# Kernel tuning notes

Hardware: AMD Instinct MI355X
Metric: run time of the kernel (lower is better)

The kernel has to match this reference:

```python
import jax, jax.numpy as jnp
import numpy as np

N_NODES = 100000
N_EDGES = 1600000
D_IN = 64
D_HID = 64
D_OUT = 64


def setup_inputs() -> dict:
    key = jax.random.key(0)
    ks = jax.random.split(key, 12)
    x = jax.random.normal(ks[0], (N_NODES, D_IN), dtype=jnp.float32)
    edge_index = jax.random.randint(ks[1], (2, N_EDGES), 0, N_NODES, dtype=jnp.int64)
    def lin(k, fan_in, fan_out):
        s = 1.0 / np.sqrt(fan_in)
        return jax.random.uniform(k, (fan_out, fan_in), jnp.float32, -s, s)
    dims = [(D_IN, D_HID), (D_HID, D_HID), (D_HID, D_OUT)]
    params = {}
    for i, (di, do) in enumerate(dims):
        params[f"W_l{i}"] = lin(ks[2 + 3 * i], di, do)      # weight for aggregated neighbors
        params[f"W_r{i}"] = lin(ks[3 + 3 * i], di, do)      # weight for root/self features
        params[f"b{i}"] = jnp.zeros((do,), jnp.float32)
    return {"x": x, "edge_index": edge_index, **params}


def _sage_conv(x, src, dst, W_l, W_r, b):
    # mean aggregation of source features at destination nodes
    agg = jax.ops.segment_sum(x[src], dst, num_segments=N_NODES)          # [N, d]
    cnt = jax.ops.segment_sum(jnp.ones_like(dst, dtype=x.dtype), dst, num_segments=N_NODES)
    mean = agg / jnp.maximum(cnt, 1.0)[:, None]
    return mean @ W_l.T + x @ W_r.T + b


def reference(x, edge_index, W_l0, W_r0, b0, W_l1, W_r1, b1, W_l2, W_r2, b2):
    src, dst = edge_index[0], edge_index[1]
    h = jax.nn.relu(_sage_conv(x, src, dst, W_l0, W_r0, b0))
    h = jax.nn.relu(_sage_conv(h, src, dst, W_l1, W_r1, b1))
    out = _sage_conv(h, src, dst, W_l2, W_r2, b2)
    return out
```

## Files before the change

### kernel.cpp

```cpp
#include <hip/hip_runtime.h>

#define N_NODES 100000
#define N_EDGES 1600000
#define D 64
#define NB 131
#define NBUCKETS 764
#define PCHUNK 8192
#define NCHUNK 196
#define PBLK 1024

typedef unsigned int u32;
typedef unsigned short u16;
typedef _Float16 f16;
typedef f16 f16x8 __attribute__((ext_vector_type(8)));
typedef float f32x4 __attribute__((ext_vector_type(4)));

__global__ __launch_bounds__(PBLK) void hist_kernel(const int* __restrict__ dst,
                                                    int* __restrict__ hist) {
    __shared__ int hcnt[NBUCKETS];
    int t = threadIdx.x;
    int c0 = blockIdx.x * PCHUNK;
    int nloc = min(PCHUNK, N_EDGES - c0);
    for (int i = t; i < NBUCKETS; i += PBLK) hcnt[i] = 0;
    __syncthreads();
    for (int i = t; i < nloc; i += PBLK) atomicAdd(&hcnt[dst[c0 + i] / NB], 1);
    __syncthreads();
    for (int i = t; i < NBUCKETS; i += PBLK) hist[blockIdx.x * NBUCKETS + i] = hcnt[i];
}

__global__ __launch_bounds__(1024) void cscan_kernel(int* __restrict__ hist,
                                                     int* __restrict__ bptr) {
    __shared__ int s[1024];
    int t = threadIdx.x;
    int tot = 0;
    if (t < NBUCKETS)
        for (int c = 0; c < NCHUNK; ++c) tot += hist[c * NBUCKETS + t];
    s[t] = tot;
    __syncthreads();
    for (int off = 1; off < 1024; off <<= 1) {
        int a = (t >= off) ? s[t - off] : 0;
        __syncthreads();
        s[t] += a;
        __syncthreads();
    }
    if (t < NBUCKETS) {
        int run = s[t] - tot;
        bptr[t] = run;
        for (int c = 0; c < NCHUNK; ++c) {
            int v = hist[c * NBUCKETS + t];
            hist[c * NBUCKETS + t] = run;
            run += v;
        }
    }
    if (t == NBUCKETS - 1) bptr[NBUCKETS] = s[t];
}

__global__ __launch_bounds__(PBLK) void part_kernel(const int* __restrict__ src,
                                                    const int* __restrict__ dst,
                                                    const int* __restrict__ cbase,
                                                    u32* __restrict__ pairs) {
    __shared__ int hcur[NBUCKETS];
    __shared__ int hb[NBUCKETS];
    int t = threadIdx.x;
    int c0 = blockIdx.x * PCHUNK;
    int nloc = min(PCHUNK, N_EDGES - c0);
    for (int i = t; i < NBUCKETS; i += PBLK) {
        hcur[i] = 0;
        hb[i] = cbase[blockIdx.x * NBUCKETS + i];
    }
    __syncthreads();
    for (int i = t; i < nloc; i += PBLK) {
        int s = src[c0 + i];
        int d = dst[c0 + i];
        int b = d / NB;
        int r = atomicAdd(&hcur[b], 1);
        pairs[hb[b] + r] = ((u32)(d - b * NB) << 24) | (u32)s;
    }
}

__global__ __launch_bounds__(256) void local_csr_kernel(
    const u32* __restrict__ pairs, const int* __restrict__ bptr,
    int* __restrict__ row_ptr, int* __restrict__ cnt, float* __restrict__ inv,
    int* __restrict__ csr_src)
{
    __shared__ int lcnt[NB];
    __shared__ int lofs[NB];
    __shared__ int s[256];

    int t = threadIdx.x, b = blockIdx.x;
    int e0 = bptr[b], e1 = bptr[b + 1];
    int nb0 = b * NB;

    for (int i = t; i < NB; i += 256) lcnt[i] = 0;
    __syncthreads();
    for (int e = e0 + t; e < e1; e += 256) atomicAdd(&lcnt[pairs[e] >> 24], 1);
    __syncthreads();

    int v = (t < NB) ? lcnt[t] : 0;
    s[t] = v;
    __syncthreads();
    for (int off = 1; off < 256; off <<= 1) {
        int a = (t >= off) ? s[t - off] : 0;
        __syncthreads();
        s[t] += a;
        __syncthreads();
    }
    if (t < NB) {
        int node = nb0 + t;
        if (node < N_NODES) {
            int excl = s[t] - v;
            lofs[t] = excl;
            row_ptr[node] = e0 + excl;
            cnt[node] = v;
            inv[node] = 1.0f / fmaxf((float)v, 1.0f);
        }
        lcnt[t] = 0;
    }
    __syncthreads();
    for (int e = e0 + t; e < e1; e += 256) {
        u32 p = pairs[e];
        int dl = (int)(p >> 24);
        int pos = atomicAdd(&lcnt[dl], 1);
        csr_src[e0 + lofs[dl] + pos] = (int)(p & 0xFFFFFFu);
    }
}

__global__ void tof16_kernel(const float* __restrict__ in, u16* __restrict__ outh, int n4) {
    int i = blockIdx.x * blockDim.x + threadIdx.x;
    if (i < n4) {
        float4 v = reinterpret_cast<const float4*>(in)[i];
        union { f16 h[4]; uint2 u; } cv;
        cv.h[0] = (f16)v.x; cv.h[1] = (f16)v.y; cv.h[2] = (f16)v.z; cv.h[3] = (f16)v.w;
        reinterpret_cast<uint2*>(outh)[i] = cv.u;
    }
}

__global__ void prep_bfrag(const float* __restrict__ Wl0, const float* __restrict__ Wr0,
                           const float* __restrict__ Wl1, const float* __restrict__ Wr1,
                           const float* __restrict__ Wl2, const float* __restrict__ Wr2,
                           uint4* __restrict__ Bfrag) {
    int idx = blockIdx.x * blockDim.x + threadIdx.x;
    if (idx >= 3 * 16 * 64) return;
    int layer = idx >> 10, r = idx & 1023, f = r >> 6, l = r & 63;
    const float* Wl = layer == 0 ? Wl0 : layer == 1 ? Wl1 : Wl2;
    const float* Wr = layer == 0 ? Wr0 : layer == 1 ? Wr1 : Wr2;
    int ktg = f >> 2, nt = f & 3;
    const float* W = (ktg & 2) ? Wr : Wl;
    int o = nt * 16 + (l & 15);
    int k = (ktg & 1) * 32 + (l >> 4) * 8;
    const float* s = W + o * 64 + k;
    float4 v0 = *reinterpret_cast<const float4*>(s);
    float4 v1 = *reinterpret_cast<const float4*>(s + 4);
    union { f16x8 h; uint4 u; } cv;
    cv.h[0] = (f16)v0.x; cv.h[1] = (f16)v0.y; cv.h[2] = (f16)v0.z; cv.h[3] = (f16)v0.w;
    cv.h[4] = (f16)v1.x; cv.h[5] = (f16)v1.y; cv.h[6] = (f16)v1.z; cv.h[7] = (f16)v1.w;
    Bfrag[idx] = cv.u;
}

__device__ __forceinline__ void add8(float* va, uint4 r) {
    union { uint4 u; f16x8 h; } cv; cv.u = r;
    #pragma unroll
    for (int e = 0; e < 8; ++e) va[e] += (float)cv.h[e];
}

__global__ __launch_bounds__(256, 8) void sage_layer(
    const u16* __restrict__ hh,
    const int* __restrict__ row_ptr, const int* __restrict__ cnt,
    const int* __restrict__ csr_src, const float* __restrict__ inv,
    const uint4* __restrict__ Bfrag,
    const float* __restrict__ bvec,
    float* __restrict__ outf,
    u16* __restrict__ outh,
    int relu)
{
    __shared__ u16 Atile[4][16][128];

    int t = threadIdx.x;
    int w    = t >> 6;
    int lane = t & 63;
    int j8   = lane & 7;
    int sg   = lane >> 3;
    const uint4* rows = reinterpret_cast<const uint4*>(hh);

    int base = blockIdx.x * 64 + w * 16;

    float bias[4];
    #pragma unroll
    for (int nt = 0; nt < 4; ++nt) bias[nt] = bvec[nt * 16 + (lane & 15)];

    #pragma unroll
    for (int slot = 0; slot < 2; ++slot) {
        int n = slot * 8 + sg;
        int node = base + n;
        bool valid = node < N_NODES;
        int nodec = valid ? node : N_NODES - 1;
        uint4 selfrow = rows[nodec * 8 + j8];
        int s0 = row_ptr[nodec];
        int c  = valid ? cnt[nodec] : 0;
        float va[8] = {0.f,0.f,0.f,0.f,0.f,0.f,0.f,0.f};
        int j = 0;
        int i0 = 0, i1 = 0, i2 = 0, i3 = 0;
        bool have = (c >= 4);
        if (have) {
            i0 = csr_src[s0];     i1 = csr_src[s0 + 1];
            i2 = csr_src[s0 + 2]; i3 = csr_src[s0 + 3];
        }
        while (have) {
            uint4 r0 = rows[i0 * 8 + j8];
            uint4 r1 = rows[i1 * 8 + j8];
            uint4 r2 = rows[i2 * 8 + j8];
            uint4 r3 = rows[i3 * 8 + j8];
            j += 4;
            have = (j + 4 <= c);
            if (have) {
                i0 = csr_src[s0 + j];     i1 = csr_src[s0 + j + 1];
                i2 = csr_src[s0 + j + 2]; i3 = csr_src[s0 + j + 3];
            }
            add8(va, r0); add8(va, r1); add8(va, r2); add8(va, r3);
        }
        for (; j < c; ++j) {
            add8(va, rows[csr_src[s0 + j] * 8 + j8]);
        }
        float sc = inv[nodec];
        union { f16x8 h; uint4 u; } mv;
        #pragma unroll
        for (int e = 0; e < 8; ++e) mv.h[e] = (f16)(va[e] * sc);
        int chunk = j8 ^ (n & 7);
        if (valid) {
            *reinterpret_cast<uint4*>(&Atile[w][n][chunk * 8]) = mv.u;
            *reinterpret_cast<uint4*>(&Atile[w][n][64 + chunk * 8]) = selfrow;
        }
    }

    f32x4 acc[4] = {};
    int row = lane & 15, kg = lane >> 4;
    #pragma unroll
    for (int ktg = 0; ktg < 4; ++ktg) {
        int idx16 = ktg * 4 + kg;
        int swz = (idx16 & 8) | ((idx16 & 7) ^ (row & 7));
        uint4 a = *reinterpret_cast<const uint4*>(&Atile[w][row][swz * 8]);
        union { uint4 u; f16x8 h; } av; av.u = a;
        #pragma unroll
        for (int nt = 0; nt < 4; ++nt) {
            union { uint4 u; f16x8 h; } bv; bv.u = Bfrag[(ktg * 4 + nt) * 64 + lane];
            acc[nt] = __builtin_amdgcn_mfma_f32_16x16x32_f16(av.h, bv.h, acc[nt], 0, 0, 0);
        }
    }

    #pragma unroll
    for (int nt = 0; nt < 4; ++nt) {
        int o = nt * 16 + (lane & 15);
        #pragma unroll
        for (int r = 0; r < 4; ++r) {
            int n = kg * 4 + r;
            int node = base + n;
            if (node < N_NODES) {
                float vout = acc[nt][r] + bias[nt];
                if (relu) vout = fmaxf(vout, 0.f);
                if (outf) outf[node * 64 + o] = vout;
                if (outh) {
                    union { f16 h; u16 u; } cv; cv.h = (f16)vout;
                    outh[node * 64 + o] = cv.u;
                }
            }
        }
    }
}

extern "C" void kernel_launch(void* const* d_in, const int* in_sizes, int n_in,
                              void* d_out, int out_size, void* d_ws, size_t ws_size,
                              hipStream_t stream) {
    const float* x   = (const float*)d_in[0];
    const int*   ei  = (const int*)d_in[1];
    const int*   src = ei;
    const int*   dst = ei + N_EDGES;
    const float* Wl0 = (const float*)d_in[2];
    const float* Wr0 = (const float*)d_in[3];
    const float* b0  = (const float*)d_in[4];
    const float* Wl1 = (const float*)d_in[5];
    const float* Wr1 = (const float*)d_in[6];
    const float* b1  = (const float*)d_in[7];
    const float* Wl2 = (const float*)d_in[8];
    const float* Wr2 = (const float*)d_in[9];
    const float* b2  = (const float*)d_in[10];
    float* out = (float*)d_out;

    char* p = (char*)d_ws;
    auto take = [&](size_t bytes) { char* r = p; p += (bytes + 255) & ~(size_t)255; return r; };
    int*   hist    = (int*)take((size_t)NCHUNK * NBUCKETS * 4);
    int*   bptr    = (int*)take((size_t)(NBUCKETS + 1) * 4);
    u32*   pairs   = (u32*)take((size_t)N_EDGES * 4);
    int*   csr_src = (int*)take((size_t)N_EDGES * 4);
    int*   row_ptr = (int*)take((size_t)N_NODES * 4);
    int*   cnt     = (int*)take((size_t)N_NODES * 4);
    float* inv     = (float*)take((size_t)N_NODES * 4);
    uint4* Bfrag   = (uint4*)take((size_t)3 * 16 * 64 * 16);
    u16*   xh      = (u16*)take((size_t)N_NODES * D * 2);
    u16*   h0h     = (u16*)take((size_t)N_NODES * D * 2);
    u16*   h1h     = (u16*)take((size_t)N_NODES * D * 2);

    const int BLK = 256;
    const int conv_grid  = (N_NODES * D / 4 + BLK - 1) / BLK;
    const int layer_grid = (N_NODES + 63) / 64;

    hist_kernel<<<NCHUNK, PBLK, 0, stream>>>(dst, hist);
    cscan_kernel<<<1, 1024, 0, stream>>>(hist, bptr);
    part_kernel<<<NCHUNK, PBLK, 0, stream>>>(src, dst, hist, pairs);
    local_csr_kernel<<<NBUCKETS, BLK, 0, stream>>>(pairs, bptr, row_ptr, cnt, inv, csr_src);
    tof16_kernel<<<conv_grid, BLK, 0, stream>>>(x, xh, N_NODES * D / 4);
    prep_bfrag<<<(3 * 1024 + BLK - 1) / BLK, BLK, 0, stream>>>(Wl0, Wr0, Wl1, Wr1, Wl2, Wr2, Bfrag);

    sage_layer<<<layer_grid, BLK, 0, stream>>>(xh,  row_ptr, cnt, csr_src, inv, Bfrag,        b0, nullptr, h0h, 1);
    sage_layer<<<layer_grid, BLK, 0, stream>>>(h0h, row_ptr, cnt, csr_src, inv, Bfrag + 1024, b1, nullptr, h1h, 1);
    sage_layer<<<layer_grid, BLK, 0, stream>>>(h1h, row_ptr, cnt, csr_src, inv, Bfrag + 2048, b2, out, nullptr, 0);
}
```

Measured before the change: 182.8 us.

## Interleave two nodes' neighbor gathers per lane and split scan into three kernels

Each lane now gathers neighbor rows for both of its nodes in one loop instead of one node after the other, so twice as many loads are in flight and memory latency is better hidden. Occupancy is lowered from 8 to 6 waves per SIMD to make room for the extra registers. The single-block column scan is split into a column-sum kernel, a bucket scan and a rebase kernel so the sums spread across several blocks, at the cost of two extra launches. Lanes whose two nodes have different degrees may leave some slots idle, and the lower occupancy could offset the gain.

```diff
diff --git a/kernel.cpp b/kernel.cpp
--- a/kernel.cpp
+++ b/kernel.cpp
@@ -28,14 +28,21 @@
     for (int i = t; i < NBUCKETS; i += PBLK) hist[blockIdx.x * NBUCKETS + i] = hcnt[i];
 }
 
-__global__ __launch_bounds__(1024) void cscan_kernel(int* __restrict__ hist,
+__global__ void colsum_kernel(const int* __restrict__ hist, int* __restrict__ btot) {
+    int t = blockIdx.x * blockDim.x + threadIdx.x;
+    if (t < NBUCKETS) {
+        int s = 0;
+        for (int c = 0; c < NCHUNK; ++c) s += hist[c * NBUCKETS + t];
+        btot[t] = s;
+    }
+}
+
+__global__ __launch_bounds__(1024) void bscan_kernel(const int* __restrict__ btot,
                                                      int* __restrict__ bptr) {
     __shared__ int s[1024];
     int t = threadIdx.x;
-    int tot = 0;
-    if (t < NBUCKETS)
-        for (int c = 0; c < NCHUNK; ++c) tot += hist[c * NBUCKETS + t];
-    s[t] = tot;
+    int v = (t < NBUCKETS) ? btot[t] : 0;
+    s[t] = v;
     __syncthreads();
     for (int off = 1; off < 1024; off <<= 1) {
         int a = (t >= off) ? s[t - off] : 0;
@@ -43,16 +50,20 @@
         s[t] += a;
         __syncthreads();
     }
+    if (t < NBUCKETS) bptr[t] = s[t] - v;
+    if (t == NBUCKETS - 1) bptr[NBUCKETS] = s[t];
+}
+
+__global__ void rebase_kernel(int* __restrict__ hist, const int* __restrict__ bptr) {
+    int t = blockIdx.x * blockDim.x + threadIdx.x;
     if (t < NBUCKETS) {
-        int run = s[t] - tot;
-        bptr[t] = run;
+        int run = bptr[t];
         for (int c = 0; c < NCHUNK; ++c) {
             int v = hist[c * NBUCKETS + t];
             hist[c * NBUCKETS + t] = run;
             run += v;
         }
     }
-    if (t == NBUCKETS - 1) bptr[NBUCKETS] = s[t];
 }
 
 __global__ __launch_bounds__(PBLK) void part_kernel(const int* __restrict__ src,
@@ -163,7 +174,7 @@
     for (int e = 0; e < 8; ++e) va[e] += (float)cv.h[e];
 }
 
-__global__ __launch_bounds__(256, 8) void sage_layer(
+__global__ __launch_bounds__(256, 6) void sage_layer(
     const u16* __restrict__ hh,
     const int* __restrict__ row_ptr, const int* __restrict__ cnt,
     const int* __restrict__ csr_src, const float* __restrict__ inv,
@@ -188,47 +199,62 @@
     #pragma unroll
     for (int nt = 0; nt < 4; ++nt) bias[nt] = bvec[nt * 16 + (lane & 15)];
 
-    #pragma unroll
-    for (int slot = 0; slot < 2; ++slot) {
-        int n = slot * 8 + sg;
-        int node = base + n;
-        bool valid = node < N_NODES;
-        int nodec = valid ? node : N_NODES - 1;
-        uint4 selfrow = rows[nodec * 8 + j8];
-        int s0 = row_ptr[nodec];
-        int c  = valid ? cnt[nodec] : 0;
-        float va[8] = {0.f,0.f,0.f,0.f,0.f,0.f,0.f,0.f};
-        int j = 0;
-        int i0 = 0, i1 = 0, i2 = 0, i3 = 0;
-        bool have = (c >= 4);
-        if (have) {
-            i0 = csr_src[s0];     i1 = csr_src[s0 + 1];
-            i2 = csr_src[s0 + 2]; i3 = csr_src[s0 + 3];
-        }
-        while (have) {
-            uint4 r0 = rows[i0 * 8 + j8];
-            uint4 r1 = rows[i1 * 8 + j8];
-            uint4 r2 = rows[i2 * 8 + j8];
-            uint4 r3 = rows[i3 * 8 + j8];
-            j += 4;
-            have = (j + 4 <= c);
-            if (have) {
-                i0 = csr_src[s0 + j];     i1 = csr_src[s0 + j + 1];
-                i2 = csr_src[s0 + j + 2]; i3 = csr_src[s0 + j + 3];
-            }
-            add8(va, r0); add8(va, r1); add8(va, r2); add8(va, r3);
-        }
-        for (; j < c; ++j) {
-            add8(va, rows[csr_src[s0 + j] * 8 + j8]);
-        }
-        float sc = inv[nodec];
+    int nA = sg, nB = 8 + sg;
+    int nodeA = base + nA, nodeB = base + nB;
+    bool validA = nodeA < N_NODES, validB = nodeB < N_NODES;
+    int nodeAc = validA ? nodeA : N_NODES - 1;
+    int nodeBc = validB ? nodeB : N_NODES - 1;
+    uint4 selfA = rows[nodeAc * 8 + j8];
+    uint4 selfB = rows[nodeBc * 8 + j8];
+    int s0A = row_ptr[nodeAc], s0B = row_ptr[nodeBc];
+    int cA = validA ? cnt[nodeAc] : 0;
+    int cB = validB ? cnt[nodeBc] : 0;
+
+    float vaA[8] = {0.f,0.f,0.f,0.f,0.f,0.f,0.f,0.f};
+    float vaB[8] = {0.f,0.f,0.f,0.f,0.f,0.f,0.f,0.f};
+    int jA = 0, jB = 0;
+    int a0 = 0, a1 = 0, a2 = 0, a3 = 0, b0 = 0, b1 = 0, b2 = 0, b3 = 0;
+    bool doA = (cA >= 4), doB = (cB >= 4);
+    if (doA) { a0 = csr_src[s0A]; a1 = csr_src[s0A + 1]; a2 = csr_src[s0A + 2]; a3 = csr_src[s0A + 3]; }
+    if (doB) { b0 = csr_src[s0B]; b1 = csr_src[s0B + 1]; b2 = csr_src[s0B + 2]; b3 = csr_src[s0B + 3]; }
+    while (__any(doA || doB)) {
+        uint4 rA0, rA1, rA2, rA3, rB0, rB1, rB2, rB3;
+        if (doA) { rA0 = rows[a0 * 8 + j8]; rA1 = rows[a1 * 8 + j8];
+                   rA2 = rows[a2 * 8 + j8]; rA3 = rows[a3 * 8 + j8]; }
+        if (doB) { rB0 = rows[b0 * 8 + j8]; rB1 = rows[b1 * 8 + j8];
+                   rB2 = rows[b2 * 8 + j8]; rB3 = rows[b3 * 8 + j8]; }
+        bool nxA = doA && (jA + 8 <= cA);
+        bool nxB = doB && (jB + 8 <= cB);
+        if (nxA) { a0 = csr_src[s0A + jA + 4]; a1 = csr_src[s0A + jA + 5];
+                   a2 = csr_src[s0A + jA + 6]; a3 = csr_src[s0A + jA + 7]; }
+        if (nxB) { b0 = csr_src[s0B + jB + 4]; b1 = csr_src[s0B + jB + 5];
+                   b2 = csr_src[s0B + jB + 6]; b3 = csr_src[s0B + jB + 7]; }
+        if (doA) { add8(vaA, rA0); add8(vaA, rA1); add8(vaA, rA2); add8(vaA, rA3); jA += 4; }
+        if (doB) { add8(vaB, rB0); add8(vaB, rB1); add8(vaB, rB2); add8(vaB, rB3); jB += 4; }
+        doA = nxA; doB = nxB;
+    }
+    for (; jA < cA; ++jA) add8(vaA, rows[csr_src[s0A + jA] * 8 + j8]);
+    for (; jB < cB; ++jB) add8(vaB, rows[csr_src[s0B + jB] * 8 + j8]);
+
+    int chunk = j8 ^ sg;
+    {
+        float sc = inv[nodeAc];
         union { f16x8 h; uint4 u; } mv;
         #pragma unroll
-        for (int e = 0; e < 8; ++e) mv.h[e] = (f16)(va[e] * sc);
-        int chunk = j8 ^ (n & 7);
-        if (valid) {
-            *reinterpret_cast<uint4*>(&Atile[w][n][chunk * 8]) = mv.u;
-            *reinterpret_cast<uint4*>(&Atile[w][n][64 + chunk * 8]) = selfrow;
+        for (int e = 0; e < 8; ++e) mv.h[e] = (f16)(vaA[e] * sc);
+        if (validA) {
+            *reinterpret_cast<uint4*>(&Atile[w][nA][chunk * 8]) = mv.u;
+            *reinterpret_cast<uint4*>(&Atile[w][nA][64 + chunk * 8]) = selfA;
+        }
+    }
+    {
+        float sc = inv[nodeBc];
+        union { f16x8 h; uint4 u; } mv;
+        #pragma unroll
+        for (int e = 0; e < 8; ++e) mv.h[e] = (f16)(vaB[e] * sc);
+        if (validB) {
+            *reinterpret_cast<uint4*>(&Atile[w][nB][chunk * 8]) = mv.u;
+            *reinterpret_cast<uint4*>(&Atile[w][nB][64 + chunk * 8]) = selfB;
         }
     }
 
@@ -288,6 +314,7 @@
     char* p = (char*)d_ws;
     auto take = [&](size_t bytes) { char* r = p; p += (bytes + 255) & ~(size_t)255; return r; };
     int*   hist    = (int*)take((size_t)NCHUNK * NBUCKETS * 4);
+    int*   btot    = (int*)take((size_t)NBUCKETS * 4);
     int*   bptr    = (int*)take((size_t)(NBUCKETS + 1) * 4);
     u32*   pairs   = (u32*)take((size_t)N_EDGES * 4);
     int*   csr_src = (int*)take((size_t)N_EDGES * 4);
@@ -302,9 +329,12 @@
     const int BLK = 256;
     const int conv_grid  = (N_NODES * D / 4 + BLK - 1) / BLK;
     const int layer_grid = (N_NODES + 63) / 64;
+    const int bgrid      = (NBUCKETS + BLK - 1) / BLK;
 
     hist_kernel<<<NCHUNK, PBLK, 0, stream>>>(dst, hist);
-    cscan_kernel<<<1, 1024, 0, stream>>>(hist, bptr);
+    colsum_kernel<<<bgrid, BLK, 0, stream>>>(hist, btot);
+    bscan_kernel<<<1, 1024, 0, stream>>>(btot, bptr);
+    rebase_kernel<<<bgrid, BLK, 0, stream>>>(hist, bptr);
     part_kernel<<<NCHUNK, PBLK, 0, stream>>>(src, dst, hist, pairs);
     local_csr_kernel<<<NBUCKETS, BLK, 0, stream>>>(pairs, bptr, row_ptr, cnt, inv, csr_src);
     tof16_kernel<<<conv_grid, BLK, 0, stream>>>(x, xh, N_NODES * D / 4);
```

After: 522.4 us. 2.86x slower.
